# Optimization experiments

Measured on AMD Instinct MI355X. Metric: run time of the kernel, lower is better.

## Reference

```python
import jax, jax.numpy as jnp
import numpy as np

N = 8192        # nodes
D_IN = 256      # in_dims
D_OUT = 32      # out_dims (assignment clusters)


def setup_inputs() -> dict:
    key = jax.random.key(0)
    k1, k2, k3 = jax.random.split(key, 3)
    main_feat = jax.random.normal(k1, (N, D_IN), dtype=jnp.float32)
    main_adj = jax.random.uniform(k2, (N, N), dtype=jnp.float32)
    W = jax.random.normal(k3, (D_IN, D_OUT), dtype=jnp.float32) * (1.0 / np.sqrt(D_IN))
    b = jnp.zeros((D_OUT,), dtype=jnp.float32)
    return {"main_feat": main_feat, "main_adj": main_adj, "W": W, "b": b}


def reference(main_feat, main_adj, W, b):
    # GraphConvolution: support = X @ W ; out = A @ support + b   -> [N, D_OUT]
    support = main_feat @ W
    assign = main_adj @ support + b
    # softmax over the NODE axis (dim 0), matching F.softmax(main_assign, 0)
    assign = jax.nn.softmax(assign, axis=0)
    # pooling: raw_emb = assign^T @ X  -> [D_OUT, D_IN]
    raw_emb = assign.T @ main_feat
    return raw_emb
```

## Files before the change

kernel.cpp:

```cpp
#include <hip/hip_runtime.h>
#include <stdint.h>

#define NN   8192
#define DIN  256
#define DOUT 32

#define PPART (NN * DOUT + 320)
#define PP4   (DOUT * DIN + 320)

typedef short bf16x8 __attribute__((ext_vector_type(8)));
typedef float f32x16 __attribute__((ext_vector_type(16)));

union BF8 { uint32_t u[4]; bf16x8 v; };

__device__ __forceinline__ void split_pair(float a, float b, uint32_t& hp, uint32_t& lp) {
    uint32_t ua = __float_as_uint(a), ub = __float_as_uint(b);
    hp = (ua >> 16) | (ub & 0xffff0000u);
    float la = a - __uint_as_float(ua & 0xffff0000u);
    float lb = b - __uint_as_float(ub & 0xffff0000u);
    lp = (__float_as_uint(la) >> 16) | (__float_as_uint(lb) & 0xffff0000u);
}

__global__ __launch_bounds__(256) void k1_support(
    const float* __restrict__ X, const float* __restrict__ W,
    unsigned short* __restrict__ hi_frag, unsigned short* __restrict__ lo_frag)
{
    __shared__ float Xs[32 * 256];
    int t = threadIdx.x;
    int kbase = blockIdx.x * 32;

    const float4* Xg = (const float4*)(X + (size_t)kbase * DIN);
    float4* Xs4 = (float4*)Xs;
#pragma unroll
    for (int p = 0; p < 8; ++p) Xs4[p * 256 + t] = Xg[p * 256 + t];
    __syncthreads();

    int c = t & 31;
    int q = t >> 5;
    int kb2  = q >> 2;
    int half = (q >> 1) & 1;
    int j4   = q & 1;
    int krow0 = kb2 * 16 + half * 8 + j4 * 4;

    float acc[4] = {0.f, 0.f, 0.f, 0.f};
    for (int d = 0; d < 256; ++d) {
        float w = W[d * 32 + c];
#pragma unroll
        for (int jj = 0; jj < 4; ++jj)
            acc[jj] += Xs[(krow0 + jj) * 256 + d] * w;
    }

    uint32_t h01, l01, h23, l23;
    split_pair(acc[0], acc[1], h01, l01);
    split_pair(acc[2], acc[3], h23, l23);

    int ks = (kbase >> 4) + kb2;
    size_t elembase = (size_t)ks * 512 + (size_t)(half * 32 + c) * 8 + j4 * 4;
    *(uint2*)(hi_frag + elembase) = make_uint2(h01, h23);
    *(uint2*)(lo_frag + elembase) = make_uint2(l01, l23);
}

__global__ __launch_bounds__(512) void k2_logits(
    const float* __restrict__ adj,
    const unsigned short* __restrict__ hi_frag,
    const unsigned short* __restrict__ lo_frag,
    float* __restrict__ part)
{
    __shared__ __align__(16) float tile[32 * 260];
    int t = threadIdx.x;
    int lane = t & 63, wv = t >> 6;
    int row0 = blockIdx.x * 32;
    size_t col0 = (size_t)blockIdx.y * 2048;

    f32x16 acc;
#pragma unroll
    for (int i = 0; i < 16; ++i) acc[i] = 0.f;

    int r  = lane & 31;
    int hs = lane >> 5;
    int tl0 = blockIdx.x & 7;

    const float* asrc = adj + (size_t)(row0 + wv) * NN + col0 + lane * 4;

    float4 pref[4];
    {
#pragma unroll
        for (int p = 0; p < 4; ++p)
            pref[p] = *(const float4*)(asrc + (size_t)(8 * p) * NN + tl0 * 256);
#pragma unroll
        for (int p = 0; p < 4; ++p)
            *(float4*)((char*)tile + (wv + 8 * p) * 1040 + lane * 16) = pref[p];
    }

    for (int tt = 0; tt < 8; ++tt) {
        int tl  = (tt + tl0) & 7;
        int tln = (tt + 1 + tl0) & 7;
        if (tt < 7) {
#pragma unroll
            for (int p = 0; p < 4; ++p)
                pref[p] = *(const float4*)(asrc + (size_t)(8 * p) * NN + tln * 256);
        }
        __syncthreads();
#pragma unroll
        for (int ss = 0; ss < 2; ++ss) {
            int s = 2 * wv + ss;
            const float4* ap = (const float4*)((const char*)tile + r * 1040 + s * 64 + hs * 32);
            float4 a0 = ap[0];
            float4 a1 = ap[1];
            int ks = (int)blockIdx.y * 128 + tl * 16 + s;
            BF8 bh, bl, ah, al;
            bh.v = *(const bf16x8*)(hi_frag + (size_t)ks * 512 + lane * 8);
            bl.v = *(const bf16x8*)(lo_frag + (size_t)ks * 512 + lane * 8);
            split_pair(a0.x, a0.y, ah.u[0], al.u[0]);
            split_pair(a0.z, a0.w, ah.u[1], al.u[1]);
            split_pair(a1.x, a1.y, ah.u[2], al.u[2]);
            split_pair(a1.z, a1.w, ah.u[3], al.u[3]);
            acc = __builtin_amdgcn_mfma_f32_32x32x16_bf16(ah.v, bh.v, acc, 0, 0, 0);
            acc = __builtin_amdgcn_mfma_f32_32x32x16_bf16(ah.v, bl.v, acc, 0, 0, 0);
            acc = __builtin_amdgcn_mfma_f32_32x32x16_bf16(al.v, bh.v, acc, 0, 0, 0);
        }
        if (tt < 7) {
            __syncthreads();
#pragma unroll
            for (int p = 0; p < 4; ++p)
                *(float4*)((char*)tile + (wv + 8 * p) * 1040 + lane * 16) = pref[p];
        }
    }

    __syncthreads();
    float* red = tile;
#pragma unroll
    for (int g = 0; g < 16; ++g) red[wv * 1024 + lane * 16 + g] = acc[g];
    __syncthreads();

    float* pdst = part + (size_t)blockIdx.y * PPART + (size_t)row0 * 32;
    for (int a = t; a < 1024; a += 512) {
        int row = a >> 5, colc = a & 31;
        int l = colc + 32 * ((row >> 2) & 1);
        int g = (row & 3) | ((row >> 3) << 2);
        float ssum = 0.f;
#pragma unroll
        for (int w8 = 0; w8 < 8; ++w8) ssum += red[w8 * 1024 + l * 16 + g];
        pdst[a] = ssum;
    }
}

__global__ __launch_bounds__(256) void t1_sum_max(
    const float* __restrict__ part, float* __restrict__ logits_sum,
    float* __restrict__ Mpart)
{
    __shared__ float red[256 * 4];
    int t = threadIdx.x;
    size_t f = (size_t)blockIdx.x * 256 + t;

    float4 v = make_float4(0.f, 0.f, 0.f, 0.f);
#pragma unroll
    for (int pp = 0; pp < 4; ++pp) {
        int p = (pp + blockIdx.x) & 3;
        float4 u = ((const float4*)(part + (size_t)p * PPART))[f];
        v.x += u.x; v.y += u.y; v.z += u.z; v.w += u.w;
    }
    ((float4*)logits_sum)[f] = v;

    red[t * 4 + 0] = v.x; red[t * 4 + 1] = v.y;
    red[t * 4 + 2] = v.z; red[t * 4 + 3] = v.w;
    __syncthreads();
    for (int s = 128; s >= 8; s >>= 1) {
        if (t < s)
#pragma unroll
            for (int j = 0; j < 4; ++j)
                red[t * 4 + j] = fmaxf(red[t * 4 + j], red[(t + s) * 4 + j]);
        __syncthreads();
    }
    if (t < 8)
#pragma unroll
        for (int j = 0; j < 4; ++j)
            Mpart[blockIdx.x * 32 + t * 4 + j] = red[t * 4 + j];
}

__global__ __launch_bounds__(256) void t2_exp_pool(
    const float* __restrict__ logits_sum, const float* __restrict__ Mpart,
    const float* __restrict__ X, float* __restrict__ Spart,
    float* __restrict__ p4)
{
    __shared__ float red[256 * 4];
    __shared__ float As[32 * 32];
    __shared__ float Xs[8 * 256];
    int t = threadIdx.x;
    int b = blockIdx.x;
    int c = t & 31, g0 = t >> 5;

    {
        float m = -3.4e38f;
#pragma unroll
        for (int gg = 0; gg < 32; ++gg)
            m = fmaxf(m, Mpart[(g0 * 32 + gg) * 32 + c]);
        red[t] = m;
    }
    __syncthreads();
    for (int s = 128; s >= 32; s >>= 1) {
        if (t < s) red[t] = fmaxf(red[t], red[t + s]);
        __syncthreads();
    }
    float m0 = red[(4 * t + 0) & 31], m1 = red[(4 * t + 1) & 31];
    float m2 = red[(4 * t + 2) & 31], m3 = red[(4 * t + 3) & 31];
    __syncthreads();

    size_t f = (size_t)b * 256 + t;
    float4 v = ((const float4*)logits_sum)[f];
    v.x = __expf(v.x - m0); v.y = __expf(v.y - m1);
    v.z = __expf(v.z - m2); v.w = __expf(v.w - m3);
    {
        int row = t >> 3, cb = (4 * t) & 31;
        As[row * 32 + cb]     = v.x;
        As[row * 32 + cb + 1] = v.y;
        As[row * 32 + cb + 2] = v.z;
        As[row * 32 + cb + 3] = v.w;
    }
    red[t * 4 + 0] = v.x; red[t * 4 + 1] = v.y;
    red[t * 4 + 2] = v.z; red[t * 4 + 3] = v.w;
    __syncthreads();
    for (int s = 128; s >= 8; s >>= 1) {
        if (t < s)
#pragma unroll
            for (int j = 0; j < 4; ++j)
                red[t * 4 + j] += red[(t + s) * 4 + j];
        __syncthreads();
    }
    if (t < 8)
#pragma unroll
        for (int j = 0; j < 4; ++j)
            Spart[b * 32 + t * 4 + j] = red[t * 4 + j];

    int dg = t >> 5;
    int ibase = b * 32;
    float acc[32];
#pragma unroll
    for (int i = 0; i < 32; ++i) acc[i] = 0.f;

    for (int rnd = 0; rnd < 4; ++rnd) {
        __syncthreads();
        const float4* Xg = (const float4*)(X + (size_t)(ibase + rnd * 8) * DIN);
        float4* Xs4 = (float4*)Xs;
        Xs4[t]       = Xg[t];
        Xs4[256 + t] = Xg[256 + t];
        __syncthreads();
#pragma unroll
        for (int i2 = 0; i2 < 8; ++i2) {
            float a = As[(rnd * 8 + i2) * 32 + c];
#pragma unroll
            for (int dd = 0; dd < 32; ++dd)
                acc[dd] += a * Xs[i2 * 256 + dg * 32 + dd];
        }
    }
    float* dst = p4 + (size_t)b * PP4 + (size_t)c * 256 + dg * 32;
#pragma unroll
    for (int q = 0; q < 8; ++q)
        ((float4*)dst)[q] = make_float4(acc[q * 4], acc[q * 4 + 1],
                                        acc[q * 4 + 2], acc[q * 4 + 3]);
}

__global__ __launch_bounds__(256) void t3_reduce(
    const float* __restrict__ p4, const float* __restrict__ Spart,
    float* __restrict__ out)
{
    __shared__ float red[256];
    __shared__ float sred[256];
    int t = threadIdx.x;
    int c_out = blockIdx.x >> 3;

    sred[t] = Spart[t * 32 + c_out];

    int j = blockIdx.x * 32 + (t & 31);
    int g0 = t >> 5;
    float a = 0.f;
#pragma unroll
    for (int gg = 0; gg < 32; ++gg) {
        int g = (g0 * 32 + gg + blockIdx.x) & 255;
        a += p4[(size_t)g * PP4 + j];
    }
    red[t] = a;
    __syncthreads();
    for (int s = 128; s >= 32; s >>= 1) {
        if (t < s) { red[t] += red[t + s]; sred[t] += sred[t + s]; }
        __syncthreads();
    }
    if (t < 32) {
        float sv = sred[t];
#pragma unroll
        for (int off = 16; off >= 1; off >>= 1) sv += __shfl_xor(sv, off);
        out[blockIdx.x * 32 + t] = red[t] / sv;
    }
}

extern "C" void kernel_launch(void* const* d_in, const int* in_sizes, int n_in,
                              void* d_out, int out_size, void* d_ws, size_t ws_size,
                              hipStream_t stream) {
    const float* X   = (const float*)d_in[0];
    const float* adj = (const float*)d_in[1];
    const float* W   = (const float*)d_in[2];
    float* out = (float*)d_out;

    char* w = (char*)d_ws;
    unsigned short* hi_frag = (unsigned short*)w;
    unsigned short* lo_frag = (unsigned short*)(w + 512 * 1024);
    size_t off = 1024 * 1024;
    float* part = (float*)(w + off);        off += (size_t)4 * PPART * sizeof(float);
    float* logits_sum = (float*)(w + off);  off += (size_t)NN * DOUT * sizeof(float);
    float* Mpart = (float*)(w + off);       off += 256 * 32 * sizeof(float);
    float* Spart = (float*)(w + off);       off += 256 * 32 * sizeof(float);
    float* p4 = (float*)(w + off);          off += (size_t)256 * PP4 * sizeof(float);

    k1_support<<<NN / 32, 256, 0, stream>>>(X, W, hi_frag, lo_frag);
    k2_logits<<<dim3(NN / 32, 4), 512, 0, stream>>>(adj, hi_frag, lo_frag, part);
    t1_sum_max<<<256, 256, 0, stream>>>(part, logits_sum, Mpart);
    t2_exp_pool<<<256, 256, 0, stream>>>(logits_sum, Mpart, X, Spart, p4);
    t3_reduce<<<256, 256, 0, stream>>>(p4, Spart, out);
}
```

Baseline: 448.2 us.

## Load adjacency directly into MFMA fragments and widen split-K to sixteen partitions

Rewrites the adjacency-by-support kernel so each wave reads its 32x16 A fragment straight from global memory instead of staging tiles through shared memory. This drops the LDS tile, the barriers and the in-block cross-wave reduction. Each wave now owns its own 32-row tile over a 512-column K slice, so there are 16 K partitions in place of 4. The reduction kernel is updated to sum 16 partial buffers, which adds partial-buffer traffic and gives less coalesced per-row 64-byte reads of the large adjacency matrix.

```diff
diff --git a/kernel.cpp b/kernel.cpp
--- a/kernel.cpp
+++ b/kernel.cpp
@@ -5,7 +5,6 @@
 #define DIN  256
 #define DOUT 32
 
-#define PPART (NN * DOUT + 320)
 #define PP4   (DOUT * DIN + 320)
 
 typedef short bf16x8 __attribute__((ext_vector_type(8)));
@@ -60,88 +59,48 @@
     *(uint2*)(lo_frag + elembase) = make_uint2(l01, l23);
 }
 
-__global__ __launch_bounds__(512) void k2_logits(
+__global__ __launch_bounds__(256) void k2_logits(
     const float* __restrict__ adj,
     const unsigned short* __restrict__ hi_frag,
     const unsigned short* __restrict__ lo_frag,
     float* __restrict__ part)
 {
-    __shared__ __align__(16) float tile[32 * 260];
     int t = threadIdx.x;
     int lane = t & 63, wv = t >> 6;
-    int row0 = blockIdx.x * 32;
-    size_t col0 = (size_t)blockIdx.y * 2048;
-
-    f32x16 acc;
-#pragma unroll
-    for (int i = 0; i < 16; ++i) acc[i] = 0.f;
-
+    int row_tile = blockIdx.x * 128 + wv * 32;
     int r  = lane & 31;
     int hs = lane >> 5;
-    int tl0 = blockIdx.x & 7;
-
-    const float* asrc = adj + (size_t)(row0 + wv) * NN + col0 + lane * 4;
-
-    float4 pref[4];
-    {
-#pragma unroll
-        for (int p = 0; p < 4; ++p)
-            pref[p] = *(const float4*)(asrc + (size_t)(8 * p) * NN + tl0 * 256);
-#pragma unroll
-        for (int p = 0; p < 4; ++p)
-            *(float4*)((char*)tile + (wv + 8 * p) * 1040 + lane * 16) = pref[p];
-    }
-
-    for (int tt = 0; tt < 8; ++tt) {
-        int tl  = (tt + tl0) & 7;
-        int tln = (tt + 1 + tl0) & 7;
-        if (tt < 7) {
-#pragma unroll
-            for (int p = 0; p < 4; ++p)
-                pref[p] = *(const float4*)(asrc + (size_t)(8 * p) * NN + tln * 256);
-        }
-        __syncthreads();
-#pragma unroll
-        for (int ss = 0; ss < 2; ++ss) {
-            int s = 2 * wv + ss;
-            const float4* ap = (const float4*)((const char*)tile + r * 1040 + s * 64 + hs * 32);
-            float4 a0 = ap[0];
-            float4 a1 = ap[1];
-            int ks = (int)blockIdx.y * 128 + tl * 16 + s;
-            BF8 bh, bl, ah, al;
-            bh.v = *(const bf16x8*)(hi_frag + (size_t)ks * 512 + lane * 8);
-            bl.v = *(const bf16x8*)(lo_frag + (size_t)ks * 512 + lane * 8);
-            split_pair(a0.x, a0.y, ah.u[0], al.u[0]);
-            split_pair(a0.z, a0.w, ah.u[1], al.u[1]);
-            split_pair(a1.x, a1.y, ah.u[2], al.u[2]);
-            split_pair(a1.z, a1.w, ah.u[3], al.u[3]);
-            acc = __builtin_amdgcn_mfma_f32_32x32x16_bf16(ah.v, bh.v, acc, 0, 0, 0);
-            acc = __builtin_amdgcn_mfma_f32_32x32x16_bf16(ah.v, bl.v, acc, 0, 0, 0);
-            acc = __builtin_amdgcn_mfma_f32_32x32x16_bf16(al.v, bh.v, acc, 0, 0, 0);
-        }
-        if (tt < 7) {
-            __syncthreads();
-#pragma unroll
-            for (int p = 0; p < 4; ++p)
-                *(float4*)((char*)tile + (wv + 8 * p) * 1040 + lane * 16) = pref[p];
-        }
-    }
-
-    __syncthreads();
-    float* red = tile;
-#pragma unroll
-    for (int g = 0; g < 16; ++g) red[wv * 1024 + lane * 16 + g] = acc[g];
-    __syncthreads();
-
-    float* pdst = part + (size_t)blockIdx.y * PPART + (size_t)row0 * 32;
-    for (int a = t; a < 1024; a += 512) {
-        int row = a >> 5, colc = a & 31;
-        int l = colc + 32 * ((row >> 2) & 1);
-        int g = (row & 3) | ((row >> 3) << 2);
-        float ssum = 0.f;
-#pragma unroll
-        for (int w8 = 0; w8 < 8; ++w8) ssum += red[w8 * 1024 + l * 16 + g];
-        pdst[a] = ssum;
+
+    const float* arow = adj + (size_t)(row_tile + r) * NN + blockIdx.y * 512 + hs * 8;
+    const unsigned short* hp = hi_frag + (size_t)blockIdx.y * 32 * 512 + lane * 8;
+    const unsigned short* lp = lo_frag + (size_t)blockIdx.y * 32 * 512 + lane * 8;
+
+    f32x16 acc;
+#pragma unroll
+    for (int i = 0; i < 16; ++i) acc[i] = 0.f;
+
+#pragma unroll 4
+    for (int s = 0; s < 32; ++s) {
+        float4 a0 = *(const float4*)arow;
+        float4 a1 = *(const float4*)(arow + 4);
+        BF8 bh, bl, ah, al;
+        bh.v = *(const bf16x8*)hp;
+        bl.v = *(const bf16x8*)lp;
+        split_pair(a0.x, a0.y, ah.u[0], al.u[0]);
+        split_pair(a0.z, a0.w, ah.u[1], al.u[1]);
+        split_pair(a1.x, a1.y, ah.u[2], al.u[2]);
+        split_pair(a1.z, a1.w, ah.u[3], al.u[3]);
+        acc = __builtin_amdgcn_mfma_f32_32x32x16_bf16(ah.v, bh.v, acc, 0, 0, 0);
+        acc = __builtin_amdgcn_mfma_f32_32x32x16_bf16(ah.v, bl.v, acc, 0, 0, 0);
+        acc = __builtin_amdgcn_mfma_f32_32x32x16_bf16(al.v, bh.v, acc, 0, 0, 0);
+        arow += 16; hp += 512; lp += 512;
+    }
+
+    float* pdst = part + (size_t)blockIdx.y * (NN * DOUT);
+#pragma unroll
+    for (int reg = 0; reg < 16; ++reg) {
+        int rt = (reg & 3) + 8 * (reg >> 2) + 4 * hs;
+        pdst[(size_t)(row_tile + rt) * 32 + r] = acc[reg];
     }
 }
 
@@ -153,11 +112,10 @@
     int t = threadIdx.x;
     size_t f = (size_t)blockIdx.x * 256 + t;
 
-    float4 v = make_float4(0.f, 0.f, 0.f, 0.f);
-#pragma unroll
-    for (int pp = 0; pp < 4; ++pp) {
-        int p = (pp + blockIdx.x) & 3;
-        float4 u = ((const float4*)(part + (size_t)p * PPART))[f];
+    float4 v = ((const float4*)part)[f];
+#pragma unroll
+    for (int p = 1; p < 16; ++p) {
+        float4 u = ((const float4*)(part + (size_t)p * NN * DOUT))[f];
         v.x += u.x; v.y += u.y; v.z += u.z; v.w += u.w;
     }
     ((float4*)logits_sum)[f] = v;
@@ -305,14 +263,14 @@
     unsigned short* hi_frag = (unsigned short*)w;
     unsigned short* lo_frag = (unsigned short*)(w + 512 * 1024);
     size_t off = 1024 * 1024;
-    float* part = (float*)(w + off);        off += (size_t)4 * PPART * sizeof(float);
+    float* part = (float*)(w + off);        off += (size_t)16 * NN * DOUT * sizeof(float);
     float* logits_sum = (float*)(w + off);  off += (size_t)NN * DOUT * sizeof(float);
     float* Mpart = (float*)(w + off);       off += 256 * 32 * sizeof(float);
     float* Spart = (float*)(w + off);       off += 256 * 32 * sizeof(float);
     float* p4 = (float*)(w + off);          off += (size_t)256 * PP4 * sizeof(float);
 
     k1_support<<<NN / 32, 256, 0, stream>>>(X, W, hi_frag, lo_frag);
-    k2_logits<<<dim3(NN / 32, 4), 512, 0, stream>>>(adj, hi_frag, lo_frag, part);
+    k2_logits<<<dim3(NN / 128, 16), 256, 0, stream>>>(adj, hi_frag, lo_frag, part);
     t1_sum_max<<<256, 256, 0, stream>>>(part, logits_sum, Mpart);
     t2_exp_pool<<<256, 256, 0, stream>>>(logits_sum, Mpart, X, Spart, p4);
     t3_reduce<<<256, 256, 0, stream>>>(p4, Spart, out);
```

Result: faster. 418.3 us (-6.7%).
